# Performance work log

Measured on AMD Instinct MI355X. Metric: run time of the kernel, lower is better.

The kernel has to match this reference:

```python
import jax, jax.numpy as jnp
import numpy as np

B, C, H, W = 4, 64, 64, 64
C8 = C // 8


def setup_inputs() -> dict:
    key = jax.random.key(0)
    ks = jax.random.split(key, 8)
    s = 1.0 / np.sqrt(C)
    return {
        "x": jax.random.normal(ks[0], (B, C, H, W), dtype=jnp.float32),
        "Wq": jax.random.normal(ks[1], (C8, C), dtype=jnp.float32) * s,
        "bq": jnp.zeros((C8,), dtype=jnp.float32),
        "Wk": jax.random.normal(ks[2], (C8, C), dtype=jnp.float32) * s,
        "bk": jnp.zeros((C8,), dtype=jnp.float32),
        "Wv": jax.random.normal(ks[3], (C, C), dtype=jnp.float32) * s,
        "bv": jnp.zeros((C,), dtype=jnp.float32),
        "gamma": jnp.zeros((1,), dtype=jnp.float32),
    }


def reference(x, Wq, bq, Wk, bk, Wv, bv, gamma):
    b, c, h, w = x.shape
    hw = h * w
    xf = x.reshape(b, c, hw)  # [B, C, HW]
    # 1x1 convs == per-pixel linear projections
    q = jnp.einsum("dc,bcn->bnd", Wq, xf) + bq            # [B, HW, C/8]
    k = jnp.einsum("dc,bcn->bdn", Wk, xf) + bk[:, None]   # [B, C/8, HW]
    v = jnp.einsum("dc,bcn->bdn", Wv, xf) + bv[:, None]   # [B, C, HW]
    scale = 1.0 / jnp.sqrt(jnp.asarray(c // 8, dtype=x.dtype))
    attn = jax.nn.softmax(jnp.einsum("bnd,bdm->bnm", q, k) * scale, axis=-1)  # [B, HW, HW]
    # out[:, :, n] = sum_m attn[n, m] * v[:, :, m]
    out = jnp.einsum("bnm,bcm->bcn", attn, v).reshape(b, c, h, w)
    return gamma[0] * out + x
```

## Files before the change

### kernel.cpp

```cpp
#include <hip/hip_runtime.h>

#define HW 4096

typedef float f32x4 __attribute__((ext_vector_type(4)));
typedef __bf16 bf16x8 __attribute__((ext_vector_type(8)));

union F8 { bf16x8 v; unsigned long long q[2]; unsigned short u[8]; __bf16 h[8]; };

__device__ inline unsigned short f2bf(float f) {
    unsigned int u = __builtin_bit_cast(unsigned int, f);
    u += 0x7fffu + ((u >> 16) & 1u);
    return (unsigned short)(u >> 16);
}
__device__ inline float bf2f(unsigned short h) {
    unsigned int u = ((unsigned int)h) << 16;
    return __builtin_bit_cast(float, u);
}
__device__ inline bf16x8 frag_lo(const unsigned short* p) {
    F8 f; f.q[0] = *(const unsigned long long*)p; f.q[1] = 0ull; return f.v;
}

#define MFMA16(a,b,c) __builtin_amdgcn_mfma_f32_16x16x32_bf16(a, b, c, 0, 0, 0)
#define EXP2(x) __builtin_amdgcn_exp2f(x)

__global__ __launch_bounds__(256, 4) void proj_kernel(
    const float* __restrict__ x,
    const float* __restrict__ Wq, const float* __restrict__ bq,
    const float* __restrict__ Wk, const float* __restrict__ bk,
    const float* __restrict__ Wv, const float* __restrict__ bv,
    unsigned short* __restrict__ qpack, unsigned short* __restrict__ kpack,
    unsigned short* __restrict__ vt3)
{
    const float A2 = 0.51006977f;
    __shared__ float ldsW[80][64];
    __shared__ float ldsB[80];

    const int blk   = blockIdx.x;
    const int b     = blk >> 8;
    const int rest  = blk & 255;
    const int ntile = rest >> 2;
    const int rg    = rest & 3;
    const int tid   = threadIdx.x;
    const int w     = tid >> 6;
    const int lane  = tid & 63;
    const int n     = ntile * 64 + lane;

#pragma unroll
    for (int kk = 0; kk < 5; ++kk) {
        const int idx = tid + kk * 256;
        const int r   = idx >> 4;
        const int c   = (idx & 15) << 2;
        f32x4 val;
        if (r < 8) { val = *(const f32x4*)(Wq + r * 64 + c); val *= A2; }
        else if (r < 16) val = *(const f32x4*)(Wk + (r - 8) * 64 + c);
        else             val = *(const f32x4*)(Wv + (r - 16) * 64 + c);
        *(f32x4*)(&ldsW[r][c]) = val;
    }
    if (tid < 80) {
        float bb = (tid < 8) ? bq[tid] * A2
                 : (tid < 16) ? bk[tid - 8] : bv[tid - 16];
        ldsB[tid] = bb;
    }
    __syncthreads();

    const float* xb = x + (size_t)b * 64 * HW + n;
    float xv[64];
#pragma unroll
    for (int c = 0; c < 64; ++c) xv[c] = xb[c * HW];

    auto rowdot = [&](int row) -> float {
        const float* wr = &ldsW[row][0];
        float a0 = 0.f, a1 = 0.f, a2 = 0.f, a3 = 0.f;
#pragma unroll
        for (int c4 = 0; c4 < 16; ++c4) {
            f32x4 wv = *(const f32x4*)(wr + c4 * 4);
            a0 = fmaf(wv[0], xv[c4*4+0], a0);
            a1 = fmaf(wv[1], xv[c4*4+1], a1);
            a2 = fmaf(wv[2], xv[c4*4+2], a2);
            a3 = fmaf(wv[3], xv[c4*4+3], a3);
        }
        return (a0 + a1) + (a2 + a3) + ldsB[row];
    };

    const int vslot = (((n >> 2) & 3) << 3) + (n & 3) + (((n >> 4) & 1) << 2);
    unsigned short* vB = vt3 + ((size_t)(b * 128 + (n >> 5)) * 64) * 32 + vslot;

    const int r0 = rg * 20 + w * 5;
#pragma unroll
    for (int rr = 0; rr < 5; ++rr) {
        const int row = r0 + rr;
        float val = rowdot(row);
        if (row < 8) {
            qpack[(size_t)(b * HW + n) * 8 + row] = f2bf(val);
        } else if (row < 16) {
            kpack[(size_t)(b * HW + n) * 8 + (row - 8)] = f2bf(val);
        } else {
            vB[(size_t)(row - 16) * 32] = f2bf(val);
        }
    }
}

__global__ __launch_bounds__(512, 1) void attn_kernel(
    const unsigned short* __restrict__ qpack,
    const unsigned short* __restrict__ kpack,
    const unsigned short* __restrict__ vt3,
    const float* __restrict__ x,
    const float* __restrict__ gamma,
    float* __restrict__ out)
{
    const int blk  = blockIdx.x;
    const int slot = blk & 7;
    const int j32  = blk >> 3;
    const int b    = slot >> 1;
    const int qt   = (j32 << 1) | (slot & 1);
    const int nb   = qt * 64;
    const int tid  = threadIdx.x;
    const int w    = tid >> 6;
    const int lane = tid & 63;
    const int g    = lane >> 4;
    const int ln   = lane & 15;

    __shared__ unsigned short ldsO[4][64][66];
    __shared__ float ldsL[8][64];

    F8 zf; zf.q[0] = 0ull; zf.q[1] = 0ull;

    bf16x8 qf[4];
#pragma unroll
    for (int i = 0; i < 4; ++i)
        qf[i] = (g == 0)
              ? frag_lo(qpack + (size_t)(b * HW + nb + 16 * i + ln) * 8)
              : zf.v;

    F8 onesu;
#pragma unroll
    for (int e = 0; e < 8; ++e) onesu.u[e] = 0x3F80;
    const bf16x8 ones = onesu.v;

    f32x4 o[4][4], ol[4];
#pragma unroll
    for (int i = 0; i < 4; ++i) {
#pragma unroll
        for (int j = 0; j < 4; ++j) o[i][j] = (f32x4){0,0,0,0};
        ol[i] = (f32x4){0,0,0,0};
    }

    const int mq = w * 512;
    const unsigned short* kb = kpack + (size_t)(b * HW + mq + ln) * 8;
    const unsigned short* vwin = vt3 + ((size_t)b * 128 + w * 16) * 2048
                               + ln * 32 + 8 * g;

#pragma unroll 2
    for (int ch = 0; ch < 16; ++ch) {
        const unsigned short* kp = kb + ch * 256;
        bf16x8 kf0 = (g == 0) ? frag_lo(kp)       : zf.v;
        bf16x8 kf1 = (g == 0) ? frag_lo(kp + 128) : zf.v;
        const unsigned short* vp = vwin + (size_t)ch * 2048;
        bf16x8 vf0 = *(const bf16x8*)(vp);
        bf16x8 vf1 = *(const bf16x8*)(vp + 512);
        bf16x8 vf2 = *(const bf16x8*)(vp + 1024);
        bf16x8 vf3 = *(const bf16x8*)(vp + 1536);

        const f32x4 z = {0.f, 0.f, 0.f, 0.f};
#pragma unroll
        for (int i = 0; i < 4; ++i) {
            f32x4 s0 = MFMA16(kf0, qf[i], z);
            f32x4 s1 = MFMA16(kf1, qf[i], z);
            F8 pa;
#pragma unroll
            for (int r = 0; r < 4; ++r) {
                pa.h[r]     = (__bf16)EXP2(s0[r]);
                pa.h[r + 4] = (__bf16)EXP2(s1[r]);
            }
            o[i][0] = MFMA16(pa.v, vf0, o[i][0]);
            o[i][1] = MFMA16(pa.v, vf1, o[i][1]);
            o[i][2] = MFMA16(pa.v, vf2, o[i][2]);
            o[i][3] = MFMA16(pa.v, vf3, o[i][3]);
            ol[i]   = MFMA16(pa.v, ones, ol[i]);
        }
    }

    if (w < 4) {
#pragma unroll
        for (int i = 0; i < 4; ++i)
#pragma unroll
            for (int r = 0; r < 4; ++r)
#pragma unroll
                for (int j = 0; j < 4; ++j)
                    ldsO[w][16 * i + 4 * g + r][16 * j + ln] = f2bf(o[i][j][r]);
    }
    if (ln == 0) {
#pragma unroll
        for (int i = 0; i < 4; ++i)
#pragma unroll
            for (int r = 0; r < 4; ++r)
                ldsL[w][16 * i + 4 * g + r] = ol[i][r];
    }
    __syncthreads();
    if (w >= 4) {
        const int s = w - 4;
#pragma unroll
        for (int i = 0; i < 4; ++i)
#pragma unroll
            for (int r = 0; r < 4; ++r)
#pragma unroll
                for (int j = 0; j < 4; ++j) {
                    unsigned short* p = &ldsO[s][16 * i + 4 * g + r][16 * j + ln];
                    *p = f2bf(bf2f(*p) + o[i][j][r]);
                }
    }
    __syncthreads();

    const int q  = tid & 63;
    const int cg = tid >> 6;
    float L = 0.f;
#pragma unroll
    for (int wv = 0; wv < 8; ++wv) L += ldsL[wv][q];
    const float inv = 1.0f / L;
    const float gm  = gamma[0];
#pragma unroll
    for (int jj = 0; jj < 8; ++jj) {
        const int c = cg + 8 * jj;
        float Ov = bf2f(ldsO[0][q][c]) + bf2f(ldsO[1][q][c])
                 + bf2f(ldsO[2][q][c]) + bf2f(ldsO[3][q][c]);
        const size_t idx = (size_t)(b * 64 + c) * HW + nb + q;
        out[idx] = fmaf(gm, Ov * inv, x[idx]);
    }
}

extern "C" void kernel_launch(void* const* d_in, const int* in_sizes, int n_in,
                              void* d_out, int out_size, void* d_ws, size_t ws_size,
                              hipStream_t stream) {
    const float* x  = (const float*)d_in[0];
    const float* Wq = (const float*)d_in[1];
    const float* bq = (const float*)d_in[2];
    const float* Wk = (const float*)d_in[3];
    const float* bk = (const float*)d_in[4];
    const float* Wv = (const float*)d_in[5];
    const float* bv = (const float*)d_in[6];
    const float* gm = (const float*)d_in[7];

    unsigned short* qpack = (unsigned short*)d_ws;
    unsigned short* kpack = qpack + 4 * HW * 8;
    unsigned short* vt3   = kpack + 4 * HW * 8;
    float* out = (float*)d_out;

    proj_kernel<<<1024, 256, 0, stream>>>(x, Wq, bq, Wk, bk, Wv, bv,
                                          qpack, kpack, vt3);
    attn_kernel<<<256, 512, 0, stream>>>(qpack, kpack, vt3, x, gm, out);
}
```

Baseline: 31.82 us.

## Split projection channel reduction across lane quarters with shuffle reduction

The projection kernel now gives each block 16 pixels instead of 64 pixels with a 4-way row split. Each lane-quarter loads 16 of the 64 input channels, and partial dot products are combined with two xor shuffles. Every thread now holds 16 x values instead of 64, which cuts register pressure and redundant x reads, and each wave handles 20 output rows. In exchange each row costs two cross-lane shuffles, global reads are only 16 pixels wide, and only one quarter of the lanes stores each row.

```diff
diff --git a/kernel.cpp b/kernel.cpp
--- a/kernel.cpp
+++ b/kernel.cpp
@@ -35,15 +35,15 @@
     __shared__ float ldsW[80][64];
     __shared__ float ldsB[80];
 
-    const int blk   = blockIdx.x;
-    const int b     = blk >> 8;
-    const int rest  = blk & 255;
-    const int ntile = rest >> 2;
-    const int rg    = rest & 3;
-    const int tid   = threadIdx.x;
-    const int w     = tid >> 6;
-    const int lane  = tid & 63;
-    const int n     = ntile * 64 + lane;
+    const int blk  = blockIdx.x;
+    const int b    = blk >> 8;
+    const int nt   = blk & 255;
+    const int tid  = threadIdx.x;
+    const int w    = tid >> 6;
+    const int lane = tid & 63;
+    const int px   = lane & 15;
+    const int qu   = lane >> 4;
+    const int n    = nt * 16 + px;
 
 #pragma unroll
     for (int kk = 0; kk < 5; ++kk) {
@@ -57,45 +57,49 @@
         *(f32x4*)(&ldsW[r][c]) = val;
     }
     if (tid < 80) {
-        float bb = (tid < 8) ? bq[tid] * A2
-                 : (tid < 16) ? bk[tid - 8] : bv[tid - 16];
-        ldsB[tid] = bb;
+        ldsB[tid] = (tid < 8) ? bq[tid] * A2
+                  : (tid < 16) ? bk[tid - 8] : bv[tid - 16];
     }
     __syncthreads();
 
-    const float* xb = x + (size_t)b * 64 * HW + n;
-    float xv[64];
-#pragma unroll
-    for (int c = 0; c < 64; ++c) xv[c] = xb[c * HW];
+    const float* xb = x + ((size_t)b * 64 + qu * 16) * HW + n;
+    float xv[16];
+#pragma unroll
+    for (int c = 0; c < 16; ++c) xv[c] = xb[(size_t)c * HW];
 
     auto rowdot = [&](int row) -> float {
-        const float* wr = &ldsW[row][0];
+        const float* wr = &ldsW[row][qu * 16];
         float a0 = 0.f, a1 = 0.f, a2 = 0.f, a3 = 0.f;
 #pragma unroll
-        for (int c4 = 0; c4 < 16; ++c4) {
+        for (int c4 = 0; c4 < 4; ++c4) {
             f32x4 wv = *(const f32x4*)(wr + c4 * 4);
             a0 = fmaf(wv[0], xv[c4*4+0], a0);
             a1 = fmaf(wv[1], xv[c4*4+1], a1);
             a2 = fmaf(wv[2], xv[c4*4+2], a2);
             a3 = fmaf(wv[3], xv[c4*4+3], a3);
         }
-        return (a0 + a1) + (a2 + a3) + ldsB[row];
+        float p = (a0 + a1) + (a2 + a3);
+        p += __shfl_xor(p, 16);
+        p += __shfl_xor(p, 32);
+        return p + ldsB[row];
     };
 
-    const int vslot = (((n >> 2) & 3) << 3) + (n & 3) + (((n >> 4) & 1) << 2);
-    unsigned short* vB = vt3 + ((size_t)(b * 128 + (n >> 5)) * 64) * 32 + vslot;
-
-    const int r0 = rg * 20 + w * 5;
-#pragma unroll
-    for (int rr = 0; rr < 5; ++rr) {
+    const int vslot = (((px >> 2) & 3) << 3) + (px & 3) + ((nt & 1) << 2);
+    unsigned short* vB = vt3 + ((size_t)(b * 128 + (nt >> 1)) * 64) * 32 + vslot;
+
+    const int r0 = w * 20;
+#pragma unroll
+    for (int rr = 0; rr < 20; ++rr) {
         const int row = r0 + rr;
         float val = rowdot(row);
-        if (row < 8) {
-            qpack[(size_t)(b * HW + n) * 8 + row] = f2bf(val);
-        } else if (row < 16) {
-            kpack[(size_t)(b * HW + n) * 8 + (row - 8)] = f2bf(val);
-        } else {
-            vB[(size_t)(row - 16) * 32] = f2bf(val);
+        if (qu == (rr & 3)) {
+            if (row < 8) {
+                qpack[(size_t)(b * HW + n) * 8 + row] = f2bf(val);
+            } else if (row < 16) {
+                kpack[(size_t)(b * HW + n) * 8 + (row - 8)] = f2bf(val);
+            } else {
+                vB[(size_t)(row - 16) * 32] = f2bf(val);
+            }
         }
     }
 }
```

Measured after the change: 32.83 us. +3.2%, slower.
